# Performance work log

Hardware: AMD Instinct MI355X
Metric: run time of the kernel (lower is better)

## Reference

```python
import jax, jax.numpy as jnp
import numpy as np

H = 64  # hidden_size
IN = 1  # input_size
OUT = 32  # fc output


def _lstm_layer(x, Wih, Whh, bih, bhh):
    """x: (B,T,D_in). Returns (outputs (B,T,H), final h (B,H)). PyTorch gate order i,f,g,o."""
    B = x.shape[0]
    b = bih + bhh  # (4H,)
    # precompute input contributions for all timesteps: (T,B,4H)
    xW = jnp.einsum('btd,gd->tbg', x, Wih) + b

    def step(carry, xw_t):
        h, c = carry
        gates = xw_t + h @ Whh.T  # (B,4H)
        i, f, g, o = jnp.split(gates, 4, axis=-1)
        i = jax.nn.sigmoid(i)
        f = jax.nn.sigmoid(f)
        g = jnp.tanh(g)
        o = jax.nn.sigmoid(o)
        c = f * c + i * g
        h = o * jnp.tanh(c)
        return (h, c), h

    h0 = jnp.zeros((B, H), dtype=x.dtype)
    c0 = jnp.zeros((B, H), dtype=x.dtype)
    (h_T, _), hs = jax.lax.scan(step, (h0, c0), xW)
    return jnp.swapaxes(hs, 0, 1), h_T


def setup_inputs() -> dict:
    key = jax.random.key(0)
    ks = jax.random.split(key, 11)
    s_ih0 = 1.0 / np.sqrt(H)
    inp = {
        'x': jax.random.normal(ks[0], (2048, 512, IN), dtype=jnp.float32),
        # layer 0: input_size -> H
        'Wih0': jax.random.uniform(ks[1], (4 * H, IN), minval=-s_ih0, maxval=s_ih0),
        'Whh0': jax.random.uniform(ks[2], (4 * H, H), minval=-s_ih0, maxval=s_ih0),
        'bih0': jax.random.uniform(ks[3], (4 * H,), minval=-s_ih0, maxval=s_ih0),
        'bhh0': jax.random.uniform(ks[4], (4 * H,), minval=-s_ih0, maxval=s_ih0),
        # layer 1: H -> H
        'Wih1': jax.random.uniform(ks[5], (4 * H, H), minval=-s_ih0, maxval=s_ih0),
        'Whh1': jax.random.uniform(ks[6], (4 * H, H), minval=-s_ih0, maxval=s_ih0),
        'bih1': jax.random.uniform(ks[7], (4 * H,), minval=-s_ih0, maxval=s_ih0),
        'bhh1': jax.random.uniform(ks[8], (4 * H,), minval=-s_ih0, maxval=s_ih0),
        # fc: H -> 32
        'fcW': jax.random.uniform(ks[9], (OUT, H), minval=-s_ih0, maxval=s_ih0),
        'fcb': jax.random.uniform(ks[10], (OUT,), minval=-s_ih0, maxval=s_ih0),
    }
    return inp


def reference(x, Wih0, Whh0, bih0, bhh0, Wih1, Whh1, bih1, bhh1, fcW, fcb):
    h1_seq, _ = _lstm_layer(x, Wih0, Whh0, bih0, bhh0)
    _, h_last = _lstm_layer(h1_seq, Wih1, Whh1, bih1, bhh1)  # hidden[-1]
    features = jax.nn.relu(h_last @ fcW.T + fcb)  # (B, 32)
    return features
```

## Files before the change

kernel.cpp:

```cpp
#include <hip/hip_runtime.h>
#include <hip/hip_bf16.h>


#define HID 64
#define TSTEPS 512
#define MB 8
#define RS 80

typedef _Float16 f16x8 __attribute__((ext_vector_type(8)));
typedef float f32x4 __attribute__((ext_vector_type(4)));

#define KSIG (-1.44269504089f)
#define KTANH (2.88539008178f)

__device__ __forceinline__ float rcp1p(float p) {
    return __builtin_amdgcn_rcpf(1.f + __builtin_amdgcn_exp2f(p));
}

#define MFMA16(A, B, C) __builtin_amdgcn_mfma_f32_16x16x32_f16((A), (B), (C), 0, 0, 0)

__global__ __launch_bounds__(512, 1) void lstm_feat_kernel(
    const float* __restrict__ x,
    const float* __restrict__ Wih0, const float* __restrict__ Whh0,
    const float* __restrict__ bih0, const float* __restrict__ bhh0,
    const float* __restrict__ Wih1, const float* __restrict__ Whh1,
    const float* __restrict__ bih1, const float* __restrict__ bhh1,
    const float* __restrict__ fcW, const float* __restrict__ fcb,
    float* __restrict__ out)
{
    __shared__ __align__(16) float x_lds[4 * TSTEPS * 2];
    __shared__ __align__(16) _Float16 h0_lds[4][MB * RS];
    __shared__ __align__(16) _Float16 h1_lds[2][MB * RS];
    __shared__ float h1f32[MB * HID];
    __shared__ float fcw_lds[HID * 32];
    __shared__ float fcb_lds[32];

    const int tid  = threadIdx.x;
    const int wave = tid >> 6;
    const int lane = tid & 63;
    const int nq   = lane & 15;
    const int quad = lane >> 4;
    const int oct  = wave * 8;
    const bool lo  = (nq < 8);
    const int bbase = blockIdx.x * MB;

    for (int i = tid; i < TSTEPS * MB; i += 512) {
        int r = i >> 9, t = i & (TSTEPS - 1);
        x_lds[(r >> 1) * (TSTEPS * 2) + t * 2 + (r & 1)] = x[(bbase + r) * TSTEPS + t];
    }
    for (int i = tid; i < 32 * HID; i += 512) {
        int o = i >> 6, kk = i & 63;
        fcw_lds[kk * 32 + o] = fcW[i];
    }
    if (tid < 32) fcb_lds[tid] = fcb[tid];
    for (int i = tid; i < 4 * MB * RS; i += 512) ((_Float16*)h0_lds)[i] = (_Float16)0.f;
    for (int i = tid; i < 2 * MB * RS; i += 512) ((_Float16*)h1_lds)[i] = (_Float16)0.f;

    f16x8 w0[2][2], wi1[2][2], wh1[2][2];
    float bs0[2], wx0[2];
    f32x4 cb1[2];
    #pragma unroll
    for (int t = 0; t < 2; ++t) {
        const int gate = 2 * t + (nq >> 3);
        const int n = gate * 64 + oct + (nq & 7);
        const float sc = (gate == 2) ? KTANH : KSIG;
        bs0[t] = (bih0[n] + bhh0[n]) * sc;
        wx0[t] = Wih0[n] * sc;
        const float cb = (bih1[n] + bhh1[n]) * sc;
        cb1[t] = (f32x4){cb, cb, cb, cb};
        #pragma unroll
        for (int ks = 0; ks < 2; ++ks) {
            const int k0 = quad * 8 + ks * 32;
            f16x8 a, b, c;
            #pragma unroll
            for (int j = 0; j < 8; ++j) {
                a[j] = (_Float16)(Whh0[n * HID + k0 + j] * sc);
                b[j] = (_Float16)(Wih1[n * HID + k0 + j] * sc);
                c[j] = (_Float16)(Whh1[n * HID + k0 + j] * sc);
            }
            w0[t][ks] = a; wi1[t][ks] = b; wh1[t][ks] = c;
        }
    }

    const int arow = (nq >> 1) * RS + quad * 8;
    const int wrow = (quad * 2 + (lo ? 0 : 1)) * RS + oct + (nq & 7);
    const int wfc  = (quad * 2 + (lo ? 0 : 1)) * HID + oct + (nq & 7);
    float cl0 = 0.f, cl1 = 0.f;

    __syncthreads();

#define L0_MM(SR, X0, X1, OUT) do {                                               \
    f16x8 a0 = *(const f16x8*)&h0_lds[SR][arow];                                  \
    f16x8 a1 = *(const f16x8*)&h0_lds[SR][arow + 32];                             \
    _Pragma("unroll")                                                             \
    for (int t = 0; t < 2; ++t) {                                                 \
        const float c0v = fmaf((X0), wx0[t], bs0[t]);                             \
        const float c1v = fmaf((X1), wx0[t], bs0[t]);                             \
        f32x4 C = {c0v, c0v, c1v, c1v};                                           \
        OUT[t] = MFMA16(a0, w0[t][0], C);                                         \
    }                                                                             \
    _Pragma("unroll")                                                             \
    for (int t = 0; t < 2; ++t) OUT[t] = MFMA16(a1, w0[t][1], OUT[t]);            \
} while (0)

#define L1_MM(S0, S1, OUT) do {                                                   \
    f16x8 p0 = *(const f16x8*)&h0_lds[S0][arow];                                  \
    f16x8 p1 = *(const f16x8*)&h0_lds[S0][arow + 32];                             \
    f16x8 q0 = *(const f16x8*)&h1_lds[S1][arow];                                  \
    f16x8 q1 = *(const f16x8*)&h1_lds[S1][arow + 32];                             \
    _Pragma("unroll")                                                             \
    for (int t = 0; t < 2; ++t) OUT[t] = MFMA16(p0, wi1[t][0], cb1[t]);           \
    _Pragma("unroll")                                                             \
    for (int t = 0; t < 2; ++t) OUT[t] = MFMA16(p1, wi1[t][1], OUT[t]);           \
    _Pragma("unroll")                                                             \
    for (int t = 0; t < 2; ++t) OUT[t] = MFMA16(q0, wh1[t][0], OUT[t]);           \
    _Pragma("unroll")                                                             \
    for (int t = 0; t < 2; ++t) OUT[t] = MFMA16(q1, wh1[t][1], OUT[t]);           \
} while (0)

#define CELLX(AC, CST, HOUT) do {                                                 \
    float r1 = __shfl_xor(lo ? AC[0][2] : AC[0][0], 8);                           \
    float r2 = __shfl_xor(lo ? AC[1][2] : AC[1][0], 8);                           \
    float pi = lo ? AC[0][0] : r1;                                                \
    float pf = lo ? r1 : AC[0][2];                                                \
    float pg = lo ? AC[1][0] : r2;                                                \
    float po = lo ? r2 : AC[1][2];                                                \
    float iv = rcp1p(pi), fv = rcp1p(pf), ov = rcp1p(po);                         \
    float gv = 1.f - 2.f * rcp1p(pg);                                             \
    CST = fmaf(fv, CST, iv * gv);                                                 \
    HOUT = ov * (1.f - 2.f * rcp1p(CST * KTANH));                                 \
} while (0)

#define IV_FULL(NM4, X0, X1) do {                                                 \
    f32x4 A0[2], A1[2];                                                           \
    __builtin_amdgcn_s_setprio(1);                                                \
    L0_MM((NM4) & 3, X0, X1, A0);                                                 \
    L1_MM(((NM4) + 3) & 3, (NM4) & 1, A1);                                        \
    __builtin_amdgcn_s_setprio(0);                                                \
    float h0v, h1v;                                                               \
    CELLX(A0, cl0, h0v);                                                          \
    h0_lds[((NM4) + 1) & 3][wrow] = (_Float16)h0v;                                \
    CELLX(A1, cl1, h1v);                                                          \
    h1_lds[((NM4) + 1) & 1][wrow] = (_Float16)h1v;                                \
    __syncthreads();                                                              \
} while (0)

#define IV_L0(NM4, X0, X1) do {                                                   \
    f32x4 A0[2];                                                                  \
    __builtin_amdgcn_s_setprio(1);                                                \
    L0_MM((NM4) & 3, X0, X1, A0);                                                 \
    __builtin_amdgcn_s_setprio(0);                                                \
    float h0v;                                                                    \
    CELLX(A0, cl0, h0v);                                                          \
    h0_lds[((NM4) + 1) & 3][wrow] = (_Float16)h0v;                                \
    __syncthreads();                                                              \
} while (0)

    const int xoff = quad * (TSTEPS * 2);

    {
        const f32x4 xv0 = *(const f32x4*)&x_lds[xoff + 0];
        const f32x4 xv1 = *(const f32x4*)&x_lds[xoff + 4];
        IV_L0(0, xv0[0], xv0[1]);
        IV_L0(1, xv0[2], xv0[3]);
        IV_FULL(2, xv1[0], xv1[1]);
        IV_FULL(3, xv1[2], xv1[3]);
    }

    for (int n = 4; n < TSTEPS; n += 4) {
        const f32x4 xv0 = *(const f32x4*)&x_lds[xoff + n * 2];
        const f32x4 xv1 = *(const f32x4*)&x_lds[xoff + n * 2 + 4];
        IV_FULL(0, xv0[0], xv0[1]);
        IV_FULL(1, xv0[2], xv0[3]);
        IV_FULL(2, xv1[0], xv1[1]);
        IV_FULL(3, xv1[2], xv1[3]);
    }

    {
        f32x4 A1[2];
        L1_MM(3, 0, A1);
        float h1v;
        CELLX(A1, cl1, h1v);
        h1_lds[1][wrow] = (_Float16)h1v;
    }
    __syncthreads();
    {
        f32x4 A1[2];
        L1_MM(0, 1, A1);
        float h1v;
        CELLX(A1, cl1, h1v);
        h1f32[wfc] = h1v;
    }
    __syncthreads();

    if (tid < MB * 32) {
        const int o  = tid & 31;
        const int rr = tid >> 5;
        float acc = fcb_lds[o];
        #pragma unroll 8
        for (int kk = 0; kk < HID; ++kk)
            acc += h1f32[rr * HID + kk] * fcw_lds[kk * 32 + o];
        out[(bbase + rr) * 32 + o] = fmaxf(acc, 0.f);
    }
}

extern "C" void kernel_launch(void* const* d_in, const int* in_sizes, int n_in,
                              void* d_out, int out_size, void* d_ws, size_t ws_size,
                              hipStream_t stream) {
    const float* x    = (const float*)d_in[0];
    const float* Wih0 = (const float*)d_in[1];
    const float* Whh0 = (const float*)d_in[2];
    const float* bih0 = (const float*)d_in[3];
    const float* bhh0 = (const float*)d_in[4];
    const float* Wih1 = (const float*)d_in[5];
    const float* Whh1 = (const float*)d_in[6];
    const float* bih1 = (const float*)d_in[7];
    const float* bhh1 = (const float*)d_in[8];
    const float* fcW  = (const float*)d_in[9];
    const float* fcb  = (const float*)d_in[10];
    float* out = (float*)d_out;

    lstm_feat_kernel<<<2048 / MB, 512, 0, stream>>>(
        x, Wih0, Whh0, bih0, bhh0, Wih1, Whh1, bih1, bhh1, fcW, fcb, out);
}
```

Baseline: 370.9 us.

## Split LSTM layers across separate wave groups with 1024-thread blocks

Doubles the block to 1024 threads so waves 0-7 run layer 0 and waves 8-15 run layer 1 concurrently, in a pipeline offset by one timestep. Until now each wave computed both layers in sequence on every step. The h0 ring buffer shrinks to two slots, and the layer-1 GEMM is split into two independent accumulator chains. The cell math is rewritten to share reciprocals, cutting the number of rcp instructions. The cost is twice as many waves contending at each per-step barrier, and the two layer groups run unbalanced amounts of work.

Measured after the change: 323.2 us. 1.15x faster.

```diff
diff --git a/kernel.cpp b/kernel.cpp
--- a/kernel.cpp
+++ b/kernel.cpp
@@ -13,13 +13,9 @@
 #define KSIG (-1.44269504089f)
 #define KTANH (2.88539008178f)
 
-__device__ __forceinline__ float rcp1p(float p) {
-    return __builtin_amdgcn_rcpf(1.f + __builtin_amdgcn_exp2f(p));
-}
-
 #define MFMA16(A, B, C) __builtin_amdgcn_mfma_f32_16x16x32_f16((A), (B), (C), 0, 0, 0)
 
-__global__ __launch_bounds__(512, 1) void lstm_feat_kernel(
+__global__ __launch_bounds__(1024, 1) void lstm_feat_kernel(
     const float* __restrict__ x,
     const float* __restrict__ Wih0, const float* __restrict__ Whh0,
     const float* __restrict__ bih0, const float* __restrict__ bhh0,
@@ -29,7 +25,7 @@
     float* __restrict__ out)
 {
     __shared__ __align__(16) float x_lds[4 * TSTEPS * 2];
-    __shared__ __align__(16) _Float16 h0_lds[4][MB * RS];
+    __shared__ __align__(16) _Float16 h0_lds[2][MB * RS];
     __shared__ __align__(16) _Float16 h1_lds[2][MB * RS];
     __shared__ float h1f32[MB * HID];
     __shared__ float fcw_lds[HID * 32];
@@ -40,21 +36,24 @@
     const int lane = tid & 63;
     const int nq   = lane & 15;
     const int quad = lane >> 4;
-    const int oct  = wave * 8;
+    const int bbase = blockIdx.x * MB;
+    const bool isL1 = (wave >= 8);
+    const int oct  = (wave & 7) * 8;
     const bool lo  = (nq < 8);
-    const int bbase = blockIdx.x * MB;
-
-    for (int i = tid; i < TSTEPS * MB; i += 512) {
+
+    for (int i = tid; i < TSTEPS * MB; i += 1024) {
         int r = i >> 9, t = i & (TSTEPS - 1);
         x_lds[(r >> 1) * (TSTEPS * 2) + t * 2 + (r & 1)] = x[(bbase + r) * TSTEPS + t];
     }
-    for (int i = tid; i < 32 * HID; i += 512) {
+    for (int i = tid; i < 32 * HID; i += 1024) {
         int o = i >> 6, kk = i & 63;
         fcw_lds[kk * 32 + o] = fcW[i];
     }
     if (tid < 32) fcb_lds[tid] = fcb[tid];
-    for (int i = tid; i < 4 * MB * RS; i += 512) ((_Float16*)h0_lds)[i] = (_Float16)0.f;
-    for (int i = tid; i < 2 * MB * RS; i += 512) ((_Float16*)h1_lds)[i] = (_Float16)0.f;
+    for (int i = tid; i < 2 * MB * RS; i += 1024) {
+        ((_Float16*)h0_lds)[i] = (_Float16)0.f;
+        ((_Float16*)h1_lds)[i] = (_Float16)0.f;
+    }
 
     f16x8 w0[2][2], wi1[2][2], wh1[2][2];
     float bs0[2], wx0[2];
@@ -64,132 +63,138 @@
         const int gate = 2 * t + (nq >> 3);
         const int n = gate * 64 + oct + (nq & 7);
         const float sc = (gate == 2) ? KTANH : KSIG;
-        bs0[t] = (bih0[n] + bhh0[n]) * sc;
-        wx0[t] = Wih0[n] * sc;
-        const float cb = (bih1[n] + bhh1[n]) * sc;
-        cb1[t] = (f32x4){cb, cb, cb, cb};
-        #pragma unroll
-        for (int ks = 0; ks < 2; ++ks) {
-            const int k0 = quad * 8 + ks * 32;
-            f16x8 a, b, c;
+        if (!isL1) {
+            bs0[t] = (bih0[n] + bhh0[n]) * sc;
+            wx0[t] = Wih0[n] * sc;
             #pragma unroll
-            for (int j = 0; j < 8; ++j) {
-                a[j] = (_Float16)(Whh0[n * HID + k0 + j] * sc);
-                b[j] = (_Float16)(Wih1[n * HID + k0 + j] * sc);
-                c[j] = (_Float16)(Whh1[n * HID + k0 + j] * sc);
+            for (int ks = 0; ks < 2; ++ks) {
+                const int k0 = quad * 8 + ks * 32;
+                f16x8 a;
+                #pragma unroll
+                for (int j = 0; j < 8; ++j)
+                    a[j] = (_Float16)(Whh0[n * HID + k0 + j] * sc);
+                w0[t][ks] = a;
             }
-            w0[t][ks] = a; wi1[t][ks] = b; wh1[t][ks] = c;
+        } else {
+            const float cb = (bih1[n] + bhh1[n]) * sc;
+            cb1[t] = (f32x4){cb, cb, cb, cb};
+            #pragma unroll
+            for (int ks = 0; ks < 2; ++ks) {
+                const int k0 = quad * 8 + ks * 32;
+                f16x8 a, b;
+                #pragma unroll
+                for (int j = 0; j < 8; ++j) {
+                    a[j] = (_Float16)(Wih1[n * HID + k0 + j] * sc);
+                    b[j] = (_Float16)(Whh1[n * HID + k0 + j] * sc);
+                }
+                wi1[t][ks] = a; wh1[t][ks] = b;
+            }
         }
     }
 
     const int arow = (nq >> 1) * RS + quad * 8;
     const int wrow = (quad * 2 + (lo ? 0 : 1)) * RS + oct + (nq & 7);
     const int wfc  = (quad * 2 + (lo ? 0 : 1)) * HID + oct + (nq & 7);
-    float cl0 = 0.f, cl1 = 0.f;
+    float cst = 0.f;
+    const f32x4 zero4 = {0.f, 0.f, 0.f, 0.f};
 
     __syncthreads();
 
-#define L0_MM(SR, X0, X1, OUT) do {                                               \
-    f16x8 a0 = *(const f16x8*)&h0_lds[SR][arow];                                  \
-    f16x8 a1 = *(const f16x8*)&h0_lds[SR][arow + 32];                             \
+#define CELL1(E00, E20, E01, E21, HOUT) do {                                      \
+    float s0 = __shfl_xor(lo ? (E20) : (E00), 8);                                 \
+    float s1 = __shfl_xor(lo ? (E21) : (E01), 8);                                 \
+    float pi = lo ? (E00) : s0;                                                   \
+    float pf = lo ? s0 : (E20);                                                   \
+    float pg = lo ? (E01) : s1;                                                   \
+    float po = lo ? s1 : (E21);                                                   \
+    float ea = __builtin_amdgcn_exp2f(pi), eb = __builtin_amdgcn_exp2f(pf);       \
+    float eg = __builtin_amdgcn_exp2f(pg), ed = __builtin_amdgcn_exp2f(po);       \
+    float Aq = ea + 1.f, Bq = eb + 1.f, Gp = eg + 1.f, Dn = ed + 1.f;             \
+    float AG = Aq * Gp;                                                           \
+    float r1 = __builtin_amdgcn_rcpf(AG * Bq);                                    \
+    cst = (cst * AG + (eg - 1.f) * Bq) * r1;                                      \
+    float E = __builtin_amdgcn_exp2f(cst * KTANH);                                \
+    float r2 = __builtin_amdgcn_rcpf(Dn * (E + 1.f));                             \
+    HOUT = (E - 1.f) * r2;                                                        \
+} while (0)
+
+#define L0_SUB(P, Q, XA, XB) do {                                                 \
+    f16x8 a0 = *(const f16x8*)&h0_lds[P][arow];                                   \
+    f16x8 a1 = *(const f16x8*)&h0_lds[P][arow + 32];                              \
+    f32x4 A[2];                                                                   \
+    __builtin_amdgcn_s_setprio(1);                                                \
     _Pragma("unroll")                                                             \
     for (int t = 0; t < 2; ++t) {                                                 \
-        const float c0v = fmaf((X0), wx0[t], bs0[t]);                             \
-        const float c1v = fmaf((X1), wx0[t], bs0[t]);                             \
-        f32x4 C = {c0v, c0v, c1v, c1v};                                           \
-        OUT[t] = MFMA16(a0, w0[t][0], C);                                         \
+        const float v0 = fmaf((XA), wx0[t], bs0[t]);                              \
+        const float v1 = fmaf((XB), wx0[t], bs0[t]);                              \
+        f32x4 C = {v0, 0.f, v1, 0.f};                                             \
+        A[t] = MFMA16(a0, w0[t][0], C);                                           \
     }                                                                             \
     _Pragma("unroll")                                                             \
-    for (int t = 0; t < 2; ++t) OUT[t] = MFMA16(a1, w0[t][1], OUT[t]);            \
+    for (int t = 0; t < 2; ++t) A[t] = MFMA16(a1, w0[t][1], A[t]);                \
+    __builtin_amdgcn_s_setprio(0);                                                \
+    float hv;                                                                     \
+    CELL1(A[0][0], A[0][2], A[1][0], A[1][2], hv);                                \
+    h0_lds[Q][wrow] = (_Float16)hv;                                               \
 } while (0)
 
-#define L1_MM(S0, S1, OUT) do {                                                   \
-    f16x8 p0 = *(const f16x8*)&h0_lds[S0][arow];                                  \
-    f16x8 p1 = *(const f16x8*)&h0_lds[S0][arow + 32];                             \
-    f16x8 q0 = *(const f16x8*)&h1_lds[S1][arow];                                  \
-    f16x8 q1 = *(const f16x8*)&h1_lds[S1][arow + 32];                             \
-    _Pragma("unroll")                                                             \
-    for (int t = 0; t < 2; ++t) OUT[t] = MFMA16(p0, wi1[t][0], cb1[t]);           \
-    _Pragma("unroll")                                                             \
-    for (int t = 0; t < 2; ++t) OUT[t] = MFMA16(p1, wi1[t][1], OUT[t]);           \
-    _Pragma("unroll")                                                             \
-    for (int t = 0; t < 2; ++t) OUT[t] = MFMA16(q0, wh1[t][0], OUT[t]);           \
-    _Pragma("unroll")                                                             \
-    for (int t = 0; t < 2; ++t) OUT[t] = MFMA16(q1, wh1[t][1], OUT[t]);           \
+#define L1_SUB(P, Q, GUARD) do {                                                  \
+    f16x8 a00 = *(const f16x8*)&h0_lds[P][arow];                                  \
+    f16x8 a01 = *(const f16x8*)&h0_lds[P][arow + 32];                             \
+    f16x8 a10 = *(const f16x8*)&h1_lds[P][arow];                                  \
+    f16x8 a11 = *(const f16x8*)&h1_lds[P][arow + 32];                             \
+    f32x4 aA[2], aB[2];                                                           \
+    __builtin_amdgcn_s_setprio(1);                                                \
+    _Pragma("unroll")                                                             \
+    for (int t = 0; t < 2; ++t) aA[t] = MFMA16(a00, wi1[t][0], zero4);            \
+    _Pragma("unroll")                                                             \
+    for (int t = 0; t < 2; ++t) aB[t] = MFMA16(a10, wh1[t][0], cb1[t]);           \
+    _Pragma("unroll")                                                             \
+    for (int t = 0; t < 2; ++t) aA[t] = MFMA16(a01, wi1[t][1], aA[t]);            \
+    _Pragma("unroll")                                                             \
+    for (int t = 0; t < 2; ++t) aB[t] = MFMA16(a11, wh1[t][1], aB[t]);            \
+    __builtin_amdgcn_s_setprio(0);                                                \
+    if (GUARD) {                                                                  \
+        float e00 = aA[0][0] + aB[0][0], e20 = aA[0][2] + aB[0][2];               \
+        float e01 = aA[1][0] + aB[1][0], e21 = aA[1][2] + aB[1][2];               \
+        float hv;                                                                 \
+        CELL1(e00, e20, e01, e21, hv);                                            \
+        h1_lds[Q][wrow] = (_Float16)hv;                                           \
+    }                                                                             \
 } while (0)
 
-#define CELLX(AC, CST, HOUT) do {                                                 \
-    float r1 = __shfl_xor(lo ? AC[0][2] : AC[0][0], 8);                           \
-    float r2 = __shfl_xor(lo ? AC[1][2] : AC[1][0], 8);                           \
-    float pi = lo ? AC[0][0] : r1;                                                \
-    float pf = lo ? r1 : AC[0][2];                                                \
-    float pg = lo ? AC[1][0] : r2;                                                \
-    float po = lo ? r2 : AC[1][2];                                                \
-    float iv = rcp1p(pi), fv = rcp1p(pf), ov = rcp1p(po);                         \
-    float gv = 1.f - 2.f * rcp1p(pg);                                             \
-    CST = fmaf(fv, CST, iv * gv);                                                 \
-    HOUT = ov * (1.f - 2.f * rcp1p(CST * KTANH));                                 \
-} while (0)
-
-#define IV_FULL(NM4, X0, X1) do {                                                 \
-    f32x4 A0[2], A1[2];                                                           \
-    __builtin_amdgcn_s_setprio(1);                                                \
-    L0_MM((NM4) & 3, X0, X1, A0);                                                 \
-    L1_MM(((NM4) + 3) & 3, (NM4) & 1, A1);                                        \
-    __builtin_amdgcn_s_setprio(0);                                                \
-    float h0v, h1v;                                                               \
-    CELLX(A0, cl0, h0v);                                                          \
-    h0_lds[((NM4) + 1) & 3][wrow] = (_Float16)h0v;                                \
-    CELLX(A1, cl1, h1v);                                                          \
-    h1_lds[((NM4) + 1) & 1][wrow] = (_Float16)h1v;                                \
-    __syncthreads();                                                              \
-} while (0)
-
-#define IV_L0(NM4, X0, X1) do {                                                   \
-    f32x4 A0[2];                                                                  \
-    __builtin_amdgcn_s_setprio(1);                                                \
-    L0_MM((NM4) & 3, X0, X1, A0);                                                 \
-    __builtin_amdgcn_s_setprio(0);                                                \
-    float h0v;                                                                    \
-    CELLX(A0, cl0, h0v);                                                          \
-    h0_lds[((NM4) + 1) & 3][wrow] = (_Float16)h0v;                                \
-    __syncthreads();                                                              \
-} while (0)
-
     const int xoff = quad * (TSTEPS * 2);
-
-    {
-        const f32x4 xv0 = *(const f32x4*)&x_lds[xoff + 0];
-        const f32x4 xv1 = *(const f32x4*)&x_lds[xoff + 4];
-        IV_L0(0, xv0[0], xv0[1]);
-        IV_L0(1, xv0[2], xv0[3]);
-        IV_FULL(2, xv1[0], xv1[1]);
-        IV_FULL(3, xv1[2], xv1[3]);
-    }
-
-    for (int n = 4; n < TSTEPS; n += 4) {
-        const f32x4 xv0 = *(const f32x4*)&x_lds[xoff + n * 2];
-        const f32x4 xv1 = *(const f32x4*)&x_lds[xoff + n * 2 + 4];
-        IV_FULL(0, xv0[0], xv0[1]);
-        IV_FULL(1, xv0[2], xv0[3]);
-        IV_FULL(2, xv1[0], xv1[1]);
-        IV_FULL(3, xv1[2], xv1[3]);
-    }
-
-    {
-        f32x4 A1[2];
-        L1_MM(3, 0, A1);
-        float h1v;
-        CELLX(A1, cl1, h1v);
-        h1_lds[1][wrow] = (_Float16)h1v;
-    }
-    __syncthreads();
-    {
-        f32x4 A1[2];
-        L1_MM(0, 1, A1);
-        float h1v;
-        CELLX(A1, cl1, h1v);
-        h1f32[wfc] = h1v;
+    for (int k = 0; k < TSTEPS; k += 2) {
+        float xa0, xa1, xb0, xb1;
+        if (!isL1) {
+            const f32x4 xv = *(const f32x4*)&x_lds[xoff + k * 2];
+            xa0 = xv[0]; xa1 = xv[1]; xb0 = xv[2]; xb1 = xv[3];
+        }
+        if (!isL1) { L0_SUB(0, 1, xa0, xa1); } else { L1_SUB(0, 1, (k > 0)); }
+        __syncthreads();
+        if (!isL1) { L0_SUB(1, 0, xb0, xb1); } else { L1_SUB(1, 0, true); }
+        __syncthreads();
+    }
+
+    if (isL1) {
+        f16x8 a00 = *(const f16x8*)&h0_lds[0][arow];
+        f16x8 a01 = *(const f16x8*)&h0_lds[0][arow + 32];
+        f16x8 a10 = *(const f16x8*)&h1_lds[0][arow];
+        f16x8 a11 = *(const f16x8*)&h1_lds[0][arow + 32];
+        f32x4 aA[2], aB[2];
+        #pragma unroll
+        for (int t = 0; t < 2; ++t) aA[t] = MFMA16(a00, wi1[t][0], zero4);
+        #pragma unroll
+        for (int t = 0; t < 2; ++t) aB[t] = MFMA16(a10, wh1[t][0], cb1[t]);
+        #pragma unroll
+        for (int t = 0; t < 2; ++t) aA[t] = MFMA16(a01, wi1[t][1], aA[t]);
+        #pragma unroll
+        for (int t = 0; t < 2; ++t) aB[t] = MFMA16(a11, wh1[t][1], aB[t]);
+        float e00 = aA[0][0] + aB[0][0], e20 = aA[0][2] + aB[0][2];
+        float e01 = aA[1][0] + aB[1][0], e21 = aA[1][2] + aB[1][2];
+        float hv;
+        CELL1(e00, e20, e01, e21, hv);
+        h1f32[wfc] = hv;
     }
     __syncthreads();
 
@@ -220,6 +225,6 @@
     const float* fcb  = (const float*)d_in[10];
     float* out = (float*)d_out;
 
-    lstm_feat_kernel<<<2048 / MB, 512, 0, stream>>>(
+    lstm_feat_kernel<<<2048 / MB, 1024, 0, stream>>>(
         x, Wih0, Whh0, bih0, bhh0, Wih1, Whh1, bih1, bhh1, fcW, fcb, out);
 }
```
